# Optimization experiments

Hardware: AMD Instinct MI355X
Metric: run time of the kernel (lower is better)

The kernel has to match this reference:

```python
import jax, jax.numpy as jnp
import numpy as np

B, N_CH, T, E = 64, 64, 1000, 512
KS = [3, 5, 7]
TC, AH, GC, HEADS, NCLS = 16, 32, 32, 4, 2
F3 = TC * len(KS)
EPS = 1e-5


def _gat(x, src, dst, W, a_src, a_dst, bias, N):
    # PyG GATConv, concat=False: h = x @ W.T -> [N, H, C]
    H, C = a_src.shape
    h = (x @ W.T).reshape(-1, H, C)
    al_s = (h * a_src).sum(-1)  # [N, H]
    al_d = (h * a_dst).sum(-1)
    e = al_s[src] + al_d[dst]  # [E, H]
    e = jnp.where(e > 0, e, 0.2 * e)  # leaky_relu(0.2)
    emax = jax.ops.segment_max(e, dst, num_segments=N)
    ex = jnp.exp(e - emax[dst])
    denom = jax.ops.segment_sum(ex, dst, num_segments=N)
    alpha = ex / denom[dst]
    out = jax.ops.segment_sum(h[src] * alpha[:, :, None], dst, num_segments=N)
    return out.mean(1) + bias  # concat=False -> head mean, then bias


def _branch(xr, cw, cb, g, b, m, v, w1, b1, w2, b2):
    k = cw.shape[-1]
    o = jax.lax.conv_general_dilated(xr, cw, (1,), [(k // 2, k // 2)],
                                     dimension_numbers=('NCH', 'OIH', 'NCH'))
    o = o + cb[None, :, None]
    o = (o - m[None, :, None]) / jnp.sqrt(v[None, :, None] + EPS) * g[None, :, None] + b[None, :, None]
    o = jax.nn.gelu(o, approximate=False)
    h = jnp.tanh(jnp.einsum('hc,nct->nht', w1, o) + b1[None, :, None])
    s = jnp.einsum('oh,nht->not', w2, h) + b2[None, :, None]  # [N,1,T]
    wts = jax.nn.softmax(s, axis=2)
    return (o * wts).sum(-1)  # [N, TC]


def reference(x, edge_index,
              conv_w_0, conv_b_0, bn_g_0, bn_b_0, bn_m_0, bn_v_0, aw1_0, ab1_0, aw2_0, ab2_0,
              conv_w_1, conv_b_1, bn_g_1, bn_b_1, bn_m_1, bn_v_1, aw1_1, ab1_1, aw2_1, ab2_1,
              conv_w_2, conv_b_2, bn_g_2, bn_b_2, bn_m_2, bn_v_2, aw1_2, ab1_2, aw2_2, ab2_2,
              se_w1, se_b1, se_w2, se_b2,
              gat1_w, gat1_asrc, gat1_adst, gat1_bias, bn1_g, bn1_b, bn1_m, bn1_v,
              skip_w, skip_b,
              gat2_w, gat2_asrc, gat2_adst, gat2_bias, bn2_g, bn2_b, bn2_m, bn2_v,
              fc_w, fc_b):
    Bx, n, Tn = x.shape
    xr = x.reshape(Bx * n, 1, Tn)
    branches = [
        (conv_w_0, conv_b_0, bn_g_0, bn_b_0, bn_m_0, bn_v_0, aw1_0, ab1_0, aw2_0, ab2_0),
        (conv_w_1, conv_b_1, bn_g_1, bn_b_1, bn_m_1, bn_v_1, aw1_1, ab1_1, aw2_1, ab2_1),
        (conv_w_2, conv_b_2, bn_g_2, bn_b_2, bn_m_2, bn_v_2, aw1_2, ab1_2, aw2_2, ab2_2),
    ]
    feats = [_branch(xr, *p) for p in branches]
    xf = jnp.concatenate(feats, axis=1)  # [B*n, F3]
    # SE block (squeeze over all nodes, per original mean over dim 0)
    sq = xf.mean(0, keepdims=True)
    sq = jax.nn.gelu(sq @ se_w1.T + se_b1, approximate=False)
    sq = jax.nn.sigmoid(sq @ se_w2.T + se_b2)
    xf = xf * sq
    # batched edge index + self loops (PyG GATConv default add_self_loops)
    offs = (jnp.arange(Bx) * n).astype(edge_index.dtype)
    src = (edge_index[0][None, :] + offs[:, None]).reshape(-1)
    dst = (edge_index[1][None, :] + offs[:, None]).reshape(-1)
    loops = jnp.arange(Bx * n, dtype=edge_index.dtype)
    src = jnp.concatenate([src, loops])
    dst = jnp.concatenate([dst, loops])
    Nn = Bx * n
    h1 = _gat(xf, src, dst, gat1_w, gat1_asrc, gat1_adst, gat1_bias, Nn)
    h1 = (h1 - bn1_m) / jnp.sqrt(bn1_v + EPS) * bn1_g + bn1_b
    h1 = jax.nn.gelu(h1 + xf @ skip_w.T + skip_b, approximate=False)
    h2 = _gat(h1, src, dst, gat2_w, gat2_asrc, gat2_adst, gat2_bias, Nn)
    h2 = (h2 - bn2_m) / jnp.sqrt(bn2_v + EPS) * bn2_g + bn2_b
    h2 = jax.nn.gelu(h2 + h1, approximate=False)
    pooled = h2.reshape(Bx, n, -1).mean(1)  # global_mean_pool per graph
    return pooled @ fc_w.T + fc_b


def setup_inputs() -> dict:
    key = jax.random.key(0)
    it = iter(jax.random.split(key, 80))
    nk = lambda *s: jax.random.normal(next(it), s, jnp.float32) * 0.1
    d = {}
    d['x'] = jax.random.normal(next(it), (B, N_CH, T), jnp.float32)
    s0 = jax.random.randint(next(it), (E,), 0, N_CH)
    off = jax.random.randint(next(it), (E,), 1, N_CH)
    d['edge_index'] = jnp.stack([s0, (s0 + off) % N_CH]).astype(jnp.int32)  # no self loops
    for i, k in enumerate(KS):
        d[f'conv_w_{i}'] = nk(TC, 1, k); d[f'conv_b_{i}'] = nk(TC)
        d[f'bn_g_{i}'] = 1.0 + nk(TC); d[f'bn_b_{i}'] = nk(TC)
        d[f'bn_m_{i}'] = nk(TC); d[f'bn_v_{i}'] = 1.0 + jnp.abs(nk(TC))
        d[f'aw1_{i}'] = nk(AH, TC); d[f'ab1_{i}'] = nk(AH)
        d[f'aw2_{i}'] = nk(1, AH); d[f'ab2_{i}'] = nk(1)
    d['se_w1'] = nk(F3 // 4, F3); d['se_b1'] = nk(F3 // 4)
    d['se_w2'] = nk(F3, F3 // 4); d['se_b2'] = nk(F3)
    d['gat1_w'] = nk(HEADS * GC, F3)
    d['gat1_asrc'] = nk(HEADS, GC); d['gat1_adst'] = nk(HEADS, GC); d['gat1_bias'] = nk(GC)
    d['bn1_g'] = 1.0 + nk(GC); d['bn1_b'] = nk(GC); d['bn1_m'] = nk(GC); d['bn1_v'] = 1.0 + jnp.abs(nk(GC))
    d['skip_w'] = nk(GC, F3); d['skip_b'] = nk(GC)
    d['gat2_w'] = nk(HEADS * GC, GC)
    d['gat2_asrc'] = nk(HEADS, GC); d['gat2_adst'] = nk(HEADS, GC); d['gat2_bias'] = nk(GC)
    d['bn2_g'] = 1.0 + nk(GC); d['bn2_b'] = nk(GC); d['bn2_m'] = nk(GC); d['bn2_v'] = 1.0 + jnp.abs(nk(GC))
    d['fc_w'] = nk(NCLS, GC); d['fc_b'] = nk(NCLS)
    return d
```

## Files before the change

### kernel.cpp

```cpp
#include <hip/hip_runtime.h>
#include <math.h>

#define N_NODES 4096
#define T_LEN 1000
#define TCH 16
#define AHD 32
#define F3D 48
#define GCD 32
#define NPG 64
#define NGRAPH 64
#define BN_EPS 1e-5f

typedef _Float16 half4_t __attribute__((ext_vector_type(4)));
typedef float float4_t __attribute__((ext_vector_type(4)));

__device__ __forceinline__ float fast_rcp(float x){ return __builtin_amdgcn_rcpf(x); }
__device__ __forceinline__ float gelu_exact(float v){
    return 0.5f*v*(1.0f+erff(v*0.70710678118654752f));
}
__device__ __forceinline__ float fast_gelu(float v){
    float av = fabsf(v);
    float z  = av*0.70710678118654752f;
    float t  = fast_rcp(1.0f + 0.3275911f*z);
    float poly = t*(0.254829592f + t*(-0.284496736f + t*(1.421413741f + t*(-1.453152027f + t*1.061405429f))));
    float ez = __builtin_amdgcn_exp2f(z*z*-1.4426950408889634f);
    float erfabs = 1.0f - poly*ez;
    return 0.5f*(v + av*erfabs);
}

struct BranchParams {
    const float* conv_w; const float* conv_b;
    const float* bn_g; const float* bn_b; const float* bn_m; const float* bn_v;
    const float* aw1; const float* ab1; const float* aw2; const float* ab2;
    int K; int col0;
};

__global__ __launch_bounds__(256)
void branch_kernel(const float* __restrict__ x,
                   BranchParams bp0, BranchParams bp1, BranchParams bp2,
                   float* __restrict__ xf)
{
    __shared__ __align__(16) float xs_f[1056];
    __shared__ __align__(8)  _Float16 xsc[4][1048];
    __shared__ __align__(8)  _Float16 cws16[256];
    __shared__ float s_arr[1024];
    __shared__ __align__(16) float shiftc[16];
    __shared__ float scl[16];
    __shared__ float redm[4], reds[4];
    __shared__ __align__(16) float fredw[4][16];

    const BranchParams bp = (blockIdx.y==0)? bp0 : (blockIdx.y==1)? bp1 : bp2;
    const int tid = threadIdx.x;
    const int node = blockIdx.x;
    const int K = bp.K;
    const float* xrow = x + (size_t)node*T_LEN;

    for (int j=tid;j<1056;j+=256){
        int q = j-8;
        xs_f[j] = (q>=0 && q<T_LEN)? xrow[q] : 0.f;
    }
    if (tid<16){
        float s = bp.bn_g[tid]*rsqrtf(bp.bn_v[tid]+BN_EPS);
        scl[tid]=s;
        shiftc[tid] = (bp.conv_b[tid]-bp.bn_m[tid])*s + bp.bn_b[tid];
    }
    __syncthreads();
    for (int j=tid;j<1048;j+=256){
        xsc[0][j]=(_Float16)xs_f[j];
        xsc[1][j]=(_Float16)xs_f[j+1];
        xsc[2][j]=(_Float16)xs_f[j+2];
        xsc[3][j]=(_Float16)xs_f[j+3];
    }
    {
        int ch=tid>>4, tap=tid&15;
        cws16[tid] = (tap<K)? (_Float16)(bp.conv_w[ch*K+tap]*scl[ch]) : (_Float16)0.f;
    }
    __syncthreads();

    const int lane = tid&63, wave = tid>>6;
    const int col  = lane&15;
    const int kg   = (lane>>4)<<2;

    const half4_t  acw = *(const half4_t*)&cws16[col*16+kg];
    const float4_t csh = *(const float4_t*)&shiftc[kg];

    float4_t wr0 = *(const float4_t*)&bp.aw1[(size_t)col*TCH + kg];
    float4_t wr1 = *(const float4_t*)&bp.aw1[(size_t)(col+16)*TCH + kg];
    half4_t a0,a1;
    #pragma unroll
    for (int r=0;r<4;r++){ a0[r]=(_Float16)wr0[r]; a1[r]=(_Float16)wr1[r]; }
    const float4_t c0  = *(const float4_t*)&bp.ab1[kg];
    const float4_t c1  = *(const float4_t*)&bp.ab1[16+kg];
    const float4_t w20 = *(const float4_t*)&bp.aw2[kg];
    const float4_t w21 = *(const float4_t*)&bp.aw2[16+kg];
    const float b2v = bp.ab2[0];
    const float w2sum8 = w20[0]+w20[1]+w20[2]+w20[3]+w21[0]+w21[1]+w21[2]+w21[3];
    const float TWO_LOG2E = 2.8853900817779268f;

    const int abase = 8 + wave*256 + col + kg - K/2;
    const int sh = abase & 3;
    const _Float16* xw_base = &xsc[sh][abase - sh];

    half4_t oreg[16];
    #pragma unroll
    for (int i=0;i<16;i++){
        half4_t xw = *(const half4_t*)(xw_base + i*16);
        float4_t d = __builtin_amdgcn_mfma_f32_16x16x16f16(acw, xw, csh, 0,0,0);
        half4_t ob;
        #pragma unroll
        for (int r=0;r<4;r++) ob[r] = (_Float16)fast_gelu(d[r]);
        oreg[i] = ob;
        float4_t h0 = __builtin_amdgcn_mfma_f32_16x16x16f16(a0, ob, c0, 0,0,0);
        float4_t h1 = __builtin_amdgcn_mfma_f32_16x16x16f16(a1, ob, c1, 0,0,0);
        float accr = 0.f;
        #pragma unroll
        for (int r=0;r<4;r++){
            accr += w20[r]*fast_rcp(__builtin_amdgcn_exp2f(h0[r]*TWO_LOG2E)+1.0f);
            accr += w21[r]*fast_rcp(__builtin_amdgcn_exp2f(h1[r]*TWO_LOG2E)+1.0f);
        }
        float part = w2sum8 - 2.0f*accr;
        part += __shfl_xor(part,16);
        part += __shfl_xor(part,32);
        const int pos0 = wave*256 + i*16;
        if (lane<16) s_arr[pos0+lane] = (pos0+lane < T_LEN)? (part + b2v) : -INFINITY;
    }
    __syncthreads();

    float sv[4];
    #pragma unroll
    for (int ii=0;ii<4;ii++) sv[ii]=s_arr[tid+ii*256];
    float m = fmaxf(fmaxf(sv[0],sv[1]),fmaxf(sv[2],sv[3]));
    #pragma unroll
    for (int off=32;off;off>>=1) m = fmaxf(m, __shfl_xor(m,off));
    if (lane==0) redm[wave]=m;
    __syncthreads();
    const float bm = fmaxf(fmaxf(redm[0],redm[1]),fmaxf(redm[2],redm[3]));
    float e[4]; float ls=0.f;
    #pragma unroll
    for (int ii=0;ii<4;ii++){ e[ii]=__expf(sv[ii]-bm); ls+=e[ii]; }
    #pragma unroll
    for (int off=32;off;off>>=1) ls += __shfl_xor(ls,off);
    if (lane==0) reds[wave]=ls;
    __syncthreads();
    const float invS = fast_rcp(reds[0]+reds[1]+reds[2]+reds[3]);
    #pragma unroll
    for (int ii=0;ii<4;ii++) s_arr[tid+ii*256]=e[ii];
    __syncthreads();

    float4_t acc = {0.f,0.f,0.f,0.f};
    #pragma unroll
    for (int i=0;i<16;i++){
        float ev = s_arr[wave*256 + i*16 + col];
        half4_t ob = oreg[i];
        #pragma unroll
        for (int r=0;r<4;r++) acc[r] += (float)ob[r]*ev;
    }
    #pragma unroll
    for (int off=1;off<16;off<<=1){
        #pragma unroll
        for (int r=0;r<4;r++) acc[r] += __shfl_xor(acc[r], off);
    }
    if (col==0) *(float4_t*)&fredw[wave][kg] = acc;
    __syncthreads();
    if (tid<16){
        float v = (fredw[0][tid]+fredw[1][tid]+fredw[2][tid]+fredw[3][tid])*invS;
        xf[(size_t)node*F3D + bp.col0 + tid] = v;
    }
}

__global__ __launch_bounds__(256)
void colsum_kernel(const float* __restrict__ xf, float* __restrict__ colmean){
    int col = blockIdx.x;
    int tid = threadIdx.x;
    float s=0.f;
    for (int i=tid;i<N_NODES;i+=256) s += xf[(size_t)i*F3D+col];
    #pragma unroll
    for (int off=32;off;off>>=1) s += __shfl_xor(s,off);
    __shared__ float red[4];
    if ((tid&63)==0) red[tid>>6]=s;
    __syncthreads();
    if (tid==0) colmean[col] = (red[0]+red[1]+red[2]+red[3])*(1.0f/(float)N_NODES);
}

__global__ __launch_bounds__(64)
void gate_kernel(const float* __restrict__ colmean,
                 const float* __restrict__ se_w1, const float* __restrict__ se_b1,
                 const float* __restrict__ se_w2, const float* __restrict__ se_b2,
                 float* __restrict__ gate){
    __shared__ float sq[F3D];
    __shared__ float g1[12];
    int tid=threadIdx.x;
    if (tid<F3D) sq[tid]=colmean[tid];
    __syncthreads();
    if (tid<12){
        float v=se_b1[tid];
        for (int j=0;j<F3D;j++) v += se_w1[tid*F3D+j]*sq[j];
        g1[tid]=gelu_exact(v);
    }
    __syncthreads();
    if (tid<F3D){
        float v=se_b2[tid];
        for (int m2=0;m2<12;m2++) v += se_w2[tid*12+m2]*g1[m2];
        gate[tid] = fast_rcp(1.0f+__expf(-v));
    }
}

__device__ __forceinline__ void edge_decode(const int* __restrict__ ei, int epg,
                                            int e, int be, int& src, int& dst){
    if (e < be){ int b=e/epg, j=e-b*epg; src=ei[j]+b*NPG; dst=ei[epg+j]+b*NPG; }
    else { src=dst=e-be; }
}

__global__ __launch_bounds__(256)
void edge_count(const int* __restrict__ ei, int epg, int* __restrict__ deg){
    int e = blockIdx.x*256+threadIdx.x;
    int be = NGRAPH*epg, total = be + N_NODES;
    if (e>=total) return;
    int s,d; edge_decode(ei,epg,e,be,s,d);
    atomicAdd(&deg[d],1);
}

__global__ __launch_bounds__(1024)
void scan_kernel(const int* __restrict__ deg, int* __restrict__ rowstart,
                 int* __restrict__ cursor){
    __shared__ int part[1024];
    int tid=threadIdx.x;
    int v0=deg[tid*4],v1=deg[tid*4+1],v2=deg[tid*4+2],v3=deg[tid*4+3];
    part[tid]=v0+v1+v2+v3;
    __syncthreads();
    for (int off=1;off<1024;off<<=1){
        int t=(tid>=off)?part[tid-off]:0;
        __syncthreads();
        part[tid]+=t;
        __syncthreads();
    }
    int base=(tid>0)?part[tid-1]:0;
    int r0=base, r1=r0+v0, r2=r1+v1, r3=r2+v2;
    rowstart[tid*4]=r0; rowstart[tid*4+1]=r1; rowstart[tid*4+2]=r2; rowstart[tid*4+3]=r3;
    cursor[tid*4]=r0;   cursor[tid*4+1]=r1;   cursor[tid*4+2]=r2;   cursor[tid*4+3]=r3;
    if (tid==1023) rowstart[4096]=part[1023];
}

__global__ __launch_bounds__(256)
void edge_fill(const int* __restrict__ ei, int epg, int* __restrict__ cursor,
               int* __restrict__ cols){
    int e = blockIdx.x*256+threadIdx.x;
    int be = NGRAPH*epg, total = be + N_NODES;
    if (e>=total) return;
    int s,d; edge_decode(ei,epg,e,be,s,d);
    int pos = atomicAdd(&cursor[d],1);
    cols[pos]=s;
}

template<int INF, bool GATED>
__global__ __launch_bounds__(128)
void gat_h_kernel(const float* __restrict__ xin_g, const float* __restrict__ gate,
                  const float* __restrict__ W,
                  const float* __restrict__ a_src, const float* __restrict__ a_dst,
                  float* __restrict__ hbuf, float* __restrict__ als, float* __restrict__ ald){
    __shared__ float xin[INF];
    __shared__ float hs[128];
    int node=blockIdx.x, tid=threadIdx.x;
    if (tid<INF){
        float v = xin_g[(size_t)node*INF+tid];
        if (GATED) v *= gate[tid];
        xin[tid]=v;
    }
    __syncthreads();
    float acc=0.f;
    const float* wr = W + (size_t)tid*INF;
    #pragma unroll
    for (int j=0;j<INF;j++) acc += wr[j]*xin[j];
    hs[tid]=acc;
    hbuf[(size_t)node*128+tid]=acc;
    __syncthreads();
    if (tid<8){
        int head=tid&3;
        const float* av = (tid<4)? a_src : a_dst;
        float s=0.f;
        for (int c=0;c<GCD;c++) s += hs[head*GCD+c]*av[head*GCD+c];
        if (tid<4) als[(size_t)node*4+head]=s;
        else       ald[(size_t)node*4+head]=s;
    }
}

__global__ __launch_bounds__(256)
void gat_gather1(const int* __restrict__ rowstart, const int* __restrict__ cols,
                 const float* __restrict__ als, const float* __restrict__ ald,
                 const float* __restrict__ hbuf,
                 const float* __restrict__ bias,
                 const float* __restrict__ bn_g, const float* __restrict__ bn_b,
                 const float* __restrict__ bn_m, const float* __restrict__ bn_v,
                 const float* __restrict__ xf, const float* __restrict__ gate,
                 const float* __restrict__ skip_w, const float* __restrict__ skip_b,
                 float* __restrict__ h1){
    const int node = blockIdx.x*8 + (threadIdx.x>>5);
    const int c = threadIdx.x&31;
    const float4 ad = ((const float4*)ald)[node];
    float n0=0,n1=0,n2=0,n3=0,d0=0,d1=0,d2=0,d3=0;
    const int s0=rowstart[node], s1=rowstart[node+1];
    for (int e=s0;e<s1;e++){
        const int src=cols[e];
        const float4 as=((const float4*)als)[src];
        float e0=as.x+ad.x; e0=e0>0.f?e0:0.2f*e0; float w0=__expf(e0);
        float e1=as.y+ad.y; e1=e1>0.f?e1:0.2f*e1; float w1=__expf(e1);
        float e2=as.z+ad.z; e2=e2>0.f?e2:0.2f*e2; float w2=__expf(e2);
        float e3=as.w+ad.w; e3=e3>0.f?e3:0.2f*e3; float w3=__expf(e3);
        const float* hr=&hbuf[(size_t)src*128];
        n0+=w0*hr[c]; n1+=w1*hr[32+c]; n2+=w2*hr[64+c]; n3+=w3*hr[96+c];
        d0+=w0; d1+=w1; d2+=w2; d3+=w3;
    }
    float acc = 0.25f*(n0*fast_rcp(d0)+n1*fast_rcp(d1)+n2*fast_rcp(d2)+n3*fast_rcp(d3)) + bias[c];
    acc = (acc-bn_m[c])*rsqrtf(bn_v[c]+BN_EPS)*bn_g[c]+bn_b[c];
    float sk = skip_b[c];
    const float* xr=&xf[(size_t)node*F3D];
    #pragma unroll
    for (int j=0;j<F3D;j++) sk += xr[j]*gate[j]*skip_w[c*F3D+j];
    h1[(size_t)node*GCD+c]=gelu_exact(acc+sk);
}

__global__ __launch_bounds__(256)
void gat_gather2(const int* __restrict__ rowstart, const int* __restrict__ cols,
                 const float* __restrict__ als, const float* __restrict__ ald,
                 const float* __restrict__ hbuf,
                 const float* __restrict__ bias,
                 const float* __restrict__ bn_g, const float* __restrict__ bn_b,
                 const float* __restrict__ bn_m, const float* __restrict__ bn_v,
                 const float* __restrict__ h1, float* __restrict__ h2){
    const int node = blockIdx.x*8 + (threadIdx.x>>5);
    const int c = threadIdx.x&31;
    const float4 ad = ((const float4*)ald)[node];
    float n0=0,n1=0,n2=0,n3=0,d0=0,d1=0,d2=0,d3=0;
    const int s0=rowstart[node], s1=rowstart[node+1];
    for (int e=s0;e<s1;e++){
        const int src=cols[e];
        const float4 as=((const float4*)als)[src];
        float e0=as.x+ad.x; e0=e0>0.f?e0:0.2f*e0; float w0=__expf(e0);
        float e1=as.y+ad.y; e1=e1>0.f?e1:0.2f*e1; float w1=__expf(e1);
        float e2=as.z+ad.z; e2=e2>0.f?e2:0.2f*e2; float w2=__expf(e2);
        float e3=as.w+ad.w; e3=e3>0.f?e3:0.2f*e3; float w3=__expf(e3);
        const float* hr=&hbuf[(size_t)src*128];
        n0+=w0*hr[c]; n1+=w1*hr[32+c]; n2+=w2*hr[64+c]; n3+=w3*hr[96+c];
        d0+=w0; d1+=w1; d2+=w2; d3+=w3;
    }
    float acc = 0.25f*(n0*fast_rcp(d0)+n1*fast_rcp(d1)+n2*fast_rcp(d2)+n3*fast_rcp(d3)) + bias[c];
    acc = (acc-bn_m[c])*rsqrtf(bn_v[c]+BN_EPS)*bn_g[c]+bn_b[c];
    float v = acc + h1[(size_t)node*GCD+c];
    h2[(size_t)node*GCD+c]=gelu_exact(v);
}

__global__ __launch_bounds__(64)
void pool_fc_kernel(const float* __restrict__ h2, const float* __restrict__ fc_w,
                    const float* __restrict__ fc_b, float* __restrict__ out){
    int g = blockIdx.x;
    int tid = threadIdx.x;
    __shared__ float part[2][GCD];
    __shared__ float pool[GCD];
    int c = tid&31, hf = tid>>5;
    float acc=0.f;
    for (int i=hf*32;i<hf*32+32;i++) acc += h2[((size_t)(g*NPG+i))*GCD+c];
    part[hf][c]=acc;
    __syncthreads();
    if (tid<GCD) pool[tid]=(part[0][tid]+part[1][tid])*(1.0f/(float)NPG);
    __syncthreads();
    if (tid<2){
        float o=fc_b[tid];
        for (int cc=0;cc<GCD;cc++) o += pool[cc]*fc_w[tid*GCD+cc];
        out[g*2+tid]=o;
    }
}

extern "C" void kernel_launch(void* const* d_in, const int* in_sizes, int n_in,
                              void* d_out, int out_size, void* d_ws, size_t ws_size,
                              hipStream_t stream){
    const float* x = (const float*)d_in[0];
    const int* ei = (const int*)d_in[1];
    const int epg = in_sizes[1]/2;

    float* ws = (float*)d_ws;
    float* xf      = ws;
    float* colmean = xf + (size_t)N_NODES*F3D;
    float* gate    = colmean + 64;
    float* hbuf    = gate + 64;
    float* als     = hbuf + (size_t)N_NODES*128;
    float* ald     = als + (size_t)N_NODES*4;
    float* h1      = ald + (size_t)N_NODES*4;
    float* h2      = h1 + (size_t)N_NODES*GCD;
    int*   deg      = (int*)(h2 + (size_t)N_NODES*GCD);
    int*   rowstart = deg + N_NODES;
    int*   cursor   = rowstart + N_NODES + 1;
    int*   cols     = cursor + N_NODES;

    auto P = [&](int i){ return (const float*)d_in[i]; };

    const int etot = NGRAPH*epg + N_NODES;
    hipMemsetAsync(deg, 0, (size_t)N_NODES*sizeof(int), stream);
    edge_count<<<(etot+255)/256,256,0,stream>>>(ei,epg,deg);
    scan_kernel<<<1,1024,0,stream>>>(deg,rowstart,cursor);
    edge_fill<<<(etot+255)/256,256,0,stream>>>(ei,epg,cursor,cols);

    BranchParams bps[3];
    const int Ks[3] = {3,5,7};
    for (int b=0;b<3;b++){
        int base = 2 + b*10;
        bps[b].conv_w = P(base+0); bps[b].conv_b = P(base+1);
        bps[b].bn_g = P(base+2);   bps[b].bn_b = P(base+3);
        bps[b].bn_m = P(base+4);   bps[b].bn_v = P(base+5);
        bps[b].aw1 = P(base+6);    bps[b].ab1 = P(base+7);
        bps[b].aw2 = P(base+8);    bps[b].ab2 = P(base+9);
        bps[b].K = Ks[b]; bps[b].col0 = b*TCH;
    }
    branch_kernel<<<dim3(N_NODES,3),256,0,stream>>>(x, bps[0], bps[1], bps[2], xf);

    colsum_kernel<<<F3D,256,0,stream>>>(xf,colmean);
    gate_kernel<<<1,64,0,stream>>>(colmean,P(32),P(33),P(34),P(35),gate);

    gat_h_kernel<F3D,true><<<N_NODES,128,0,stream>>>(xf,gate,P(36),P(37),P(38),hbuf,als,ald);
    gat_gather1<<<N_NODES/8,256,0,stream>>>(rowstart,cols,als,ald,hbuf,
                                            P(39),P(40),P(41),P(42),P(43),
                                            xf,gate,P(44),P(45),h1);

    gat_h_kernel<GCD,false><<<N_NODES,128,0,stream>>>(h1,nullptr,P(46),P(47),P(48),hbuf,als,ald);
    gat_gather2<<<N_NODES/8,256,0,stream>>>(rowstart,cols,als,ald,hbuf,
                                            P(49),P(50),P(51),P(52),P(53),
                                            h1,h2);

    pool_fc_kernel<<<NGRAPH,64,0,stream>>>(h2,P(54),P(55),(float*)d_out);
}
```

Before: 263.5 us.

## Cheapen GELU and tanh math with shared reciprocals; merge colsum and gate kernels

Replaces the erf-polynomial GELU with a sigmoid-form approximation, v/(1+exp2(poly*v)), and pairs two reciprocals into one by multiplying the denominators. The 2*log2(e) scale of the tanh attention layer is folded into the fp16 MFMA weights and biases, which removes a multiply per element, and the tanh sigmoids are likewise paired to share one rcp. The colsum and gate kernels become a single 1024-thread block, saving one launch but reducing the column reduction to one workgroup. The aim is fewer transcendental ops in the hot branch kernel. The cost is some accuracy from the GELU approximation, fp16 rounding of the scaled weights, and a serial reduction.

Result: slower. 320.6 us (+21.7%).

```diff
diff --git a/kernel.cpp b/kernel.cpp
--- a/kernel.cpp
+++ b/kernel.cpp
@@ -17,15 +17,6 @@
 __device__ __forceinline__ float fast_rcp(float x){ return __builtin_amdgcn_rcpf(x); }
 __device__ __forceinline__ float gelu_exact(float v){
     return 0.5f*v*(1.0f+erff(v*0.70710678118654752f));
-}
-__device__ __forceinline__ float fast_gelu(float v){
-    float av = fabsf(v);
-    float z  = av*0.70710678118654752f;
-    float t  = fast_rcp(1.0f + 0.3275911f*z);
-    float poly = t*(0.254829592f + t*(-0.284496736f + t*(1.421413741f + t*(-1.453152027f + t*1.061405429f))));
-    float ez = __builtin_amdgcn_exp2f(z*z*-1.4426950408889634f);
-    float erfabs = 1.0f - poly*ez;
-    return 0.5f*(v + av*erfabs);
 }
 
 struct BranchParams {
@@ -84,18 +75,24 @@
     const half4_t  acw = *(const half4_t*)&cws16[col*16+kg];
     const float4_t csh = *(const float4_t*)&shiftc[kg];
 
+    const float TWO_LOG2E = 2.8853900817779268f;
+
     float4_t wr0 = *(const float4_t*)&bp.aw1[(size_t)col*TCH + kg];
     float4_t wr1 = *(const float4_t*)&bp.aw1[(size_t)(col+16)*TCH + kg];
     half4_t a0,a1;
     #pragma unroll
-    for (int r=0;r<4;r++){ a0[r]=(_Float16)wr0[r]; a1[r]=(_Float16)wr1[r]; }
-    const float4_t c0  = *(const float4_t*)&bp.ab1[kg];
-    const float4_t c1  = *(const float4_t*)&bp.ab1[16+kg];
+    for (int r=0;r<4;r++){ a0[r]=(_Float16)(wr0[r]*TWO_LOG2E); a1[r]=(_Float16)(wr1[r]*TWO_LOG2E); }
+    float4_t c0  = *(const float4_t*)&bp.ab1[kg];
+    float4_t c1  = *(const float4_t*)&bp.ab1[16+kg];
+    #pragma unroll
+    for (int r=0;r<4;r++){ c0[r]*=TWO_LOG2E; c1[r]*=TWO_LOG2E; }
     const float4_t w20 = *(const float4_t*)&bp.aw2[kg];
     const float4_t w21 = *(const float4_t*)&bp.aw2[16+kg];
     const float b2v = bp.ab2[0];
     const float w2sum8 = w20[0]+w20[1]+w20[2]+w20[3]+w21[0]+w21[1]+w21[2]+w21[3];
-    const float TWO_LOG2E = 2.8853900817779268f;
+
+    const float C1GE = -2.30220818f;
+    const float C2GE = -0.10294324f;
 
     const int abase = 8 + wave*256 + col + kg - K/2;
     const int sh = abase & 3;
@@ -106,19 +103,40 @@
     for (int i=0;i<16;i++){
         half4_t xw = *(const half4_t*)(xw_base + i*16);
         float4_t d = __builtin_amdgcn_mfma_f32_16x16x16f16(acw, xw, csh, 0,0,0);
+
+        float vv[4], dd[4];
+        #pragma unroll
+        for (int r=0;r<4;r++){
+            float v = d[r];
+            vv[r] = v;
+            float t = fmaxf(v, -9.0f);
+            float u = t*t;
+            float pq = fmaf(C2GE, u, C1GE);
+            dd[r] = __builtin_amdgcn_exp2f(pq*t) + 1.0f;
+        }
         half4_t ob;
-        #pragma unroll
-        for (int r=0;r<4;r++) ob[r] = (_Float16)fast_gelu(d[r]);
+        {
+            float rp0 = fast_rcp(dd[0]*dd[1]);
+            float rp1 = fast_rcp(dd[2]*dd[3]);
+            ob[0] = (_Float16)(vv[0]*(dd[1]*rp0));
+            ob[1] = (_Float16)(vv[1]*(dd[0]*rp0));
+            ob[2] = (_Float16)(vv[2]*(dd[3]*rp1));
+            ob[3] = (_Float16)(vv[3]*(dd[2]*rp1));
+        }
         oreg[i] = ob;
+
         float4_t h0 = __builtin_amdgcn_mfma_f32_16x16x16f16(a0, ob, c0, 0,0,0);
         float4_t h1 = __builtin_amdgcn_mfma_f32_16x16x16f16(a1, ob, c1, 0,0,0);
         float accr = 0.f;
         #pragma unroll
         for (int r=0;r<4;r++){
-            accr += w20[r]*fast_rcp(__builtin_amdgcn_exp2f(h0[r]*TWO_LOG2E)+1.0f);
-            accr += w21[r]*fast_rcp(__builtin_amdgcn_exp2f(h1[r]*TWO_LOG2E)+1.0f);
+            float e0 = __builtin_amdgcn_exp2f(h0[r]) + 1.0f;
+            float e1 = __builtin_amdgcn_exp2f(h1[r]) + 1.0f;
+            float rp = fast_rcp(e0*e1);
+            accr = fmaf(w20[r], e1*rp, accr);
+            accr = fmaf(w21[r], e0*rp, accr);
         }
-        float part = w2sum8 - 2.0f*accr;
+        float part = fmaf(-2.0f, accr, w2sum8);
         part += __shfl_xor(part,16);
         part += __shfl_xor(part,32);
         const int pos0 = wave*256 + i*16;
@@ -168,33 +186,26 @@
     }
 }
 
-__global__ __launch_bounds__(256)
-void colsum_kernel(const float* __restrict__ xf, float* __restrict__ colmean){
-    int col = blockIdx.x;
-    int tid = threadIdx.x;
-    float s=0.f;
-    for (int i=tid;i<N_NODES;i+=256) s += xf[(size_t)i*F3D+col];
-    #pragma unroll
-    for (int off=32;off;off>>=1) s += __shfl_xor(s,off);
-    __shared__ float red[4];
-    if ((tid&63)==0) red[tid>>6]=s;
-    __syncthreads();
-    if (tid==0) colmean[col] = (red[0]+red[1]+red[2]+red[3])*(1.0f/(float)N_NODES);
-}
-
-__global__ __launch_bounds__(64)
-void gate_kernel(const float* __restrict__ colmean,
-                 const float* __restrict__ se_w1, const float* __restrict__ se_b1,
-                 const float* __restrict__ se_w2, const float* __restrict__ se_b2,
-                 float* __restrict__ gate){
-    __shared__ float sq[F3D];
+__global__ __launch_bounds__(1024)
+void colgate_kernel(const float* __restrict__ xf,
+                    const float* __restrict__ se_w1, const float* __restrict__ se_b1,
+                    const float* __restrict__ se_w2, const float* __restrict__ se_b2,
+                    float* __restrict__ gate){
+    __shared__ float cm[F3D];
     __shared__ float g1[12];
-    int tid=threadIdx.x;
-    if (tid<F3D) sq[tid]=colmean[tid];
+    const int tid = threadIdx.x;
+    const int wave = tid>>6, lane = tid&63;
+    for (int c = wave; c < F3D; c += 16){
+        float s = 0.f;
+        for (int r = lane; r < N_NODES; r += 64) s += xf[(size_t)r*F3D + c];
+        #pragma unroll
+        for (int off=32;off;off>>=1) s += __shfl_xor(s,off);
+        if (lane==0) cm[c] = s*(1.0f/(float)N_NODES);
+    }
     __syncthreads();
     if (tid<12){
         float v=se_b1[tid];
-        for (int j=0;j<F3D;j++) v += se_w1[tid*F3D+j]*sq[j];
+        for (int j=0;j<F3D;j++) v += se_w1[tid*F3D+j]*cm[j];
         g1[tid]=gelu_exact(v);
     }
     __syncthreads();
@@ -379,8 +390,7 @@
 
     float* ws = (float*)d_ws;
     float* xf      = ws;
-    float* colmean = xf + (size_t)N_NODES*F3D;
-    float* gate    = colmean + 64;
+    float* gate    = xf + (size_t)N_NODES*F3D;
     float* hbuf    = gate + 64;
     float* als     = hbuf + (size_t)N_NODES*128;
     float* ald     = als + (size_t)N_NODES*4;
@@ -412,8 +422,7 @@
     }
     branch_kernel<<<dim3(N_NODES,3),256,0,stream>>>(x, bps[0], bps[1], bps[2], xf);
 
-    colsum_kernel<<<F3D,256,0,stream>>>(xf,colmean);
-    gate_kernel<<<1,64,0,stream>>>(colmean,P(32),P(33),P(34),P(35),gate);
+    colgate_kernel<<<1,1024,0,stream>>>(xf,P(32),P(33),P(34),P(35),gate);
 
     gat_h_kernel<F3D,true><<<N_NODES,128,0,stream>>>(xf,gate,P(36),P(37),P(38),hbuf,als,ald);
     gat_gather1<<<N_NODES/8,256,0,stream>>>(rowstart,cols,als,ald,hbuf,
```
